# Kernel tuning notes

Hardware: AMD Instinct MI355X
Metric: run time of the kernel (lower is better)

## Reference

```python
import jax, jax.numpy as jnp
import numpy as np

K = 3          # patch_size
PAD = 1        # (K-1)//2
EPS = 1e-8
STYLE_STRENGTH = 1.0


def _whiten(x):
    # WCT whitening: zero-mean, multiply by Cov^{-1/2} (eigendecomposition)
    B, C, H, W = x.shape
    f = x.reshape(B, C, H * W)
    f = f - f.mean(-1, keepdims=True)
    cov = jnp.einsum('bcn,bdn->bcd', f, f) / (H * W - 1)
    e, v = jnp.linalg.eigh(cov)
    d = 1.0 / jnp.sqrt(jnp.maximum(e, EPS))
    wmat = jnp.einsum('bce,be,bde->bcd', v, d, v)   # V diag(e^-1/2) V^T
    return jnp.einsum('bcd,bdn->bcn', wmat, f).reshape(B, C, H, W)


def _color(x, target):
    # WCT coloring: multiply by style Cov^{1/2}, add style mean
    B, C, H, W = x.shape
    f = x.reshape(B, C, H * W)
    t = target.reshape(B, C, -1)
    tm = t.mean(-1, keepdims=True)
    tc = t - tm
    cov = jnp.einsum('bcn,bdn->bcd', tc, tc) / (tc.shape[-1] - 1)
    e, v = jnp.linalg.eigh(cov)
    d = jnp.sqrt(jnp.maximum(e, 0.0))
    cmat = jnp.einsum('bce,be,bde->bcd', v, d, v)   # V diag(e^1/2) V^T
    out = jnp.einsum('bcd,bdn->bcn', cmat, f) + tm
    return out.reshape(B, C, H, W)


def _extract_patches(x):
    # [B,C,H,W] -> [B,H*W,C,K*K], zero padding, stride 1 (matches torch unfold order)
    B, C, H, W = x.shape
    xp = jnp.pad(x, ((0, 0), (0, 0), (PAD, PAD), (PAD, PAD)))
    pats = jnp.stack([xp[:, :, i:i + H, j:j + W] for i in range(K) for j in range(K)], axis=-1)
    return pats.reshape(B, C, H * W, K * K).transpose(0, 2, 1, 3)


def _style_decorator(content_feature, style_feature):
    nc = _whiten(content_feature)
    ns = _whiten(style_feature)
    B, C, H, W = nc.shape
    P = ns.shape[2] * ns.shape[3]                     # number of style patches
    kern = _extract_patches(ns).reshape(B, P, C * K * K)
    knorm = jnp.linalg.norm(kern, axis=2, keepdims=True) + 1e-5
    cpat = _extract_patches(nc).reshape(B, H * W, C * K * K)
    # conv2d with normalized style kernels == cosine-similarity cross-correlation
    score = jnp.einsum('bqm,bpm->bpq', cpat, kern / knorm)    # [B, P, H*W]
    # binarization_patch_score: per-pixel argmax over style patches (one-hot),
    # then deconv with UNNORMALIZED kernels == gather the winning kernel per pixel
    idx = jnp.argmax(score, axis=1)                           # [B, H*W]
    gathered = jnp.take_along_axis(kern, idx[:, :, None], axis=1)  # [B, H*W, C*K*K]
    G = gathered.reshape(B, H, W, C, K, K).transpose(0, 3, 1, 2, 4, 5)  # [B,C,H,W,K,K]
    # conv_transpose2d(pad=K-1) on zero-padded one-hot == overlap-add of kernels
    full = jnp.zeros((B, C, H + K - 1, W + K - 1), dtype=nc.dtype)
    for dx in range(K):
        for dy in range(K):
            full = full.at[:, :, dx:dx + H, dy:dy + W].add(G[..., dx, dy])
    out = full[:, :, PAD:PAD + H, PAD:PAD + W]
    # norm_deconvolution: overlap counts (static)
    nfull = np.zeros((H + K - 1, W + K - 1), dtype=np.float32)
    for dx in range(K):
        for dy in range(K):
            nfull[dx:dx + H, dy:dy + W] += 1.0
    dn = jnp.asarray(nfull[PAD:PAD + H, PAD:PAD + W])
    reassembled = out / dn
    stylized = _color(reassembled, style_feature)
    return (1.0 - STYLE_STRENGTH) * content_feature + STYLE_STRENGTH * stylized


def setup_inputs() -> dict:
    key = jax.random.key(0)
    k1, k2 = jax.random.split(key)
    return {
        'content_feature': jax.random.normal(k1, (2, 512, 64, 64), dtype=jnp.float32),
        'style_feature': jax.random.normal(k2, (2, 512, 64, 64), dtype=jnp.float32),
    }


def reference(content_feature, style_feature):
    return _style_decorator(content_feature, style_feature)
```

## Files before the change

kernel.cpp:

```cpp
#include <hip/hip_runtime.h>


#define CH    512
#define NPIX  4096
#define HPAD  66
#define PPAD  4356
#define MROWS 4480
#define BANDW 2304
#define BANDOFF 2112
#define NS_ITERS 7

typedef unsigned short u16;
typedef _Float16 half8 __attribute__((ext_vector_type(8)));
typedef __attribute__((ext_vector_type(4))) float f32x4;

__device__ __forceinline__ float f16tof(u16 h){
  union { u16 u; _Float16 f; } v; v.u = h; return (float)v.f;
}
__device__ __forceinline__ void split2(float x, u16& h, u16& l){
  _Float16 hf = (_Float16)x;
  float r = (x - (float)hf) * 2048.0f;
  union { u16 u; _Float16 f; } hv, lv;
  hv.f = hf; lv.f = (_Float16)r;
  h = hv.u; l = lv.u;
}
__device__ __forceinline__ void gll16(const void* g, void* l){
  __builtin_amdgcn_global_load_lds((const __attribute__((address_space(1))) unsigned*)g,
                                   (__attribute__((address_space(3))) unsigned*)l,
                                   16, 0, 0);
}
__device__ __forceinline__ f32x4 mfma_f16(half8 a, half8 b, f32x4 c){
  return __builtin_amdgcn_mfma_f32_16x16x32_f16(a, b, c, 0, 0, 0);
}

enum { M_COVP = 0, M_NST = 1, M_X3 = 2, M_WHITEN = 3, M_S0 = 4, M_COLOR = 5 };

struct GP {
  const u16 *Ah, *Al, *Bh, *Bl;
  const u16 *Eh, *El, *Fh, *Fl;
  size_t sAz, sBz;
  float* Cf;
  u16 *Ch, *Cl;
  u16 *Gh, *Gl;
  size_t sCz;
  const float* scales;
  const float* meanv;
  int K;
  int Kit;
};

template<int TILE, int MODE>
__global__ __launch_bounds__(256, 2)
void gemm_sp(GP p){
  constexpr int MF = TILE / 32;
  constexpr bool SYM = (MODE == M_NST) || (MODE == M_X3);
  const int z = blockIdx.z;
  int m0, n0;
  int kbase = 0;
  int za = z, zout = z;
  bool mirror = false;
  if constexpr (MODE == M_COVP){
    const int b = blockIdx.x;
    const int xcd = b & 7, w = b >> 3;
    const int zc = xcd*2 + (w & 1);
    const int tile = w >> 1;
    m0 = (tile >> 3)*64; n0 = (tile & 7)*64;
    kbase = (zc & 3) * p.Kit;
    za = zc >> 2; zout = zc;
  } else if constexpr (SYM){
    int bx = blockIdx.x;
    int ty = 0;
    while((ty+1)*(ty+2)/2 <= bx) ++ty;
    int tx = bx - ty*(ty+1)/2;
    m0 = ty*64; n0 = tx*64; mirror = (tx != ty);
  } else if constexpr (MODE == M_S0){
    const int b = blockIdx.x;
    const int v = (b & 7)*79 + (b >> 3);
    if(v >= 630) return;
    m0 = (v / 18)*128; n0 = (v % 18)*128;
  } else {
    m0 = blockIdx.y*TILE; n0 = blockIdx.x*TILE;
  }

  const u16 *Ah, *Al, *Bh, *Bl;
  if constexpr (MODE == M_X3){
    const size_t zb = (size_t)(z & 3) * CH * CH;
    if(z < 4){ Ah=p.Ah+zb; Al=p.Al+zb; Bh=p.Bh+zb; Bl=p.Bl+zb; }
    else     { Ah=p.Eh+zb; Al=p.El+zb; Bh=p.Fh+zb; Bl=p.Fl+zb; }
  } else {
    Ah = p.Ah + (size_t)za * p.sAz;
    Al = p.Al + (size_t)za * p.sAz;
    Bh = p.Bh + (size_t)za * p.sBz;
    Bl = p.Bl + (size_t)za * p.sBz;
  }

  const int tid = threadIdx.x, ln = tid & 63, wv = tid >> 6;
  const int wm = (wv >> 1) * (TILE/2), wn = (wv & 1) * (TILE/2);
  __shared__ __align__(16) u16 sAh[2][TILE*32], sAl[2][TILE*32];
  __shared__ __align__(16) u16 sBh[2][TILE*32], sBl[2][TILE*32];
  f32x4 acc1[MF][MF], acc2[MF][MF];
#pragma unroll
  for(int i=0;i<MF;++i)
#pragma unroll
    for(int j=0;j<MF;++j){ acc1[i][j] = (f32x4)0.0f; acc2[i][j] = (f32x4)0.0f; }
  const int K = p.K;

  auto stage = [&](int k0, int buf){
#pragma unroll
    for(int s = tid; s < TILE*4; s += 256){
      const int row = s >> 2, pos = s & 3;
      const int kc = pos ^ ((row >> 2) & 3);
      const size_t ga = (size_t)(m0 + row) * K + k0 + kc*8;
      const size_t gb = (size_t)(n0 + row) * K + k0 + kc*8;
      gll16(Ah + ga, sAh[buf] + s*8);
      gll16(Al + ga, sAl[buf] + s*8);
      gll16(Bh + gb, sBh[buf] + s*8);
      gll16(Bl + gb, sBl[buf] + s*8);
    }
  };

  stage(kbase, 0);
  int cur = 0;
  for(int kk = 0; kk < p.Kit; kk += 32){
    __syncthreads();
    if(kk + 32 < p.Kit) stage(kbase + kk + 32, cur ^ 1);
    const u16* pAh = sAh[cur]; const u16* pAl = sAl[cur];
    const u16* pBh = sBh[cur]; const u16* pBl = sBl[cur];
    half8 ah[MF], al[MF], bh[MF], bl[MF];
#pragma unroll
    for(int i=0;i<MF;++i){
      const int ra = wm + i*16 + (ln & 15);
      const int rb = wn + i*16 + (ln & 15);
      const int pa = (ln >> 4) ^ ((ra >> 2) & 3);
      const int pb = (ln >> 4) ^ ((rb >> 2) & 3);
      const int ofa = ra*32 + pa*8;
      const int ofb = rb*32 + pb*8;
      ah[i] = *(const half8*)(pAh + ofa);
      al[i] = *(const half8*)(pAl + ofa);
      bh[i] = *(const half8*)(pBh + ofb);
      bl[i] = *(const half8*)(pBl + ofb);
    }
#pragma unroll
    for(int i=0;i<MF;++i)
#pragma unroll
      for(int j=0;j<MF;++j){
        acc1[i][j] = mfma_f16(ah[i], bh[j], acc1[i][j]);
        acc2[i][j] = mfma_f16(ah[i], bl[j], acc2[i][j]);
        acc2[i][j] = mfma_f16(al[i], bh[j], acc2[i][j]);
      }
    cur ^= 1;
  }
  u16 *C0 = nullptr, *C1 = nullptr;
  if constexpr (MODE == M_NST){
    const size_t zb = (size_t)z * p.sCz;
    C0 = p.Ch + zb; C1 = p.Cl + zb;
  } else if constexpr (MODE == M_X3){
    const size_t zb = (size_t)(z & 3) * p.sCz;
    if(z < 4){ C0 = p.Ch + zb; C1 = p.Cl + zb; }
    else     { C0 = p.Gh + zb; C1 = p.Gl + zb; }
  }
#pragma unroll
  for(int i=0;i<MF;++i)
#pragma unroll
    for(int j=0;j<MF;++j)
#pragma unroll
      for(int r=0;r<4;++r){
        const int m = m0 + wm + i*16 + (ln >> 4)*4 + r;
        const int n = n0 + wn + j*16 + (ln & 15);
        float v = acc1[i][j][r] + acc2[i][j][r] * (1.0f/2048.0f);
        if constexpr (MODE == M_COVP){
          p.Cf[(size_t)zout * p.sCz + (size_t)m * CH + n] = v;
        } else if constexpr (MODE == M_NST || MODE == M_X3){
          if constexpr (MODE == M_NST) v = -0.5f*v + ((m == n) ? 1.5f : 0.0f);
          u16 h, l; split2(v, h, l);
          C0[(size_t)m*CH + n] = h; C1[(size_t)m*CH + n] = l;
          if(mirror){
            C0[(size_t)n*CH + m] = h; C1[(size_t)n*CH + m] = l;
          }
        } else if constexpr (MODE == M_WHITEN){
          v *= p.scales[z*4 + 3];
          const int prow = ((m >> 6) + 1)*HPAD + (m & 63) + 1;
          u16 h, l; split2(v, h, l);
          const size_t o = (size_t)z*p.sCz + (size_t)prow*CH + n;
          p.Ch[o] = h; p.Cl[o] = l;
        } else if constexpr (MODE == M_S0){
          p.Cf[(size_t)m * BANDW + n] = v;
        } else {
          const float sc = p.scales[(2+z)*4 + 2];
          const float mu = p.meanv[(2+z)*CH + m];
          p.Cf[(size_t)z*p.sCz + (size_t)m*NPIX + n] = v*sc + mu;
        }
      }
}

__global__ __launch_bounds__(256)
void cov_reduce_kernel(const float* __restrict__ covp, float* __restrict__ cov){
  size_t t = (size_t)blockIdx.x * 256 + threadIdx.x;
  int z = (int)(t >> 18);
  size_t e = t & 262143;
  float s = 0.f;
#pragma unroll
  for(int c = 0; c < 4; ++c) s += covp[((size_t)(z*4 + c) << 18) + e];
  cov[t] = s * (1.0f / 4095.0f);
}

__global__ __launch_bounds__(256)
void scale_pre_kernel(const float* __restrict__ cov, int* __restrict__ cmax){
  const int z = blockIdx.y;
  const int col = blockIdx.x * 256 + threadIdx.x;
  const float* C = cov + (size_t)z * CH * CH;
  float s = 0.f;
  for(int r = 0; r < CH; ++r) s += fabsf(C[(size_t)r * CH + col]);
  atomicMax(&cmax[z], __float_as_int(s));
}
__global__ __launch_bounds__(64)
void scale_fin_kernel(const int* __restrict__ cmax, float* __restrict__ scales){
  int z = threadIdx.x;
  if(z < 4){
    float c = __int_as_float(cmax[z]);
    scales[z*4+0] = c;
    scales[z*4+1] = 1.0f / c;
    scales[z*4+2] = sqrtf(c);
    scales[z*4+3] = rsqrtf(c);
  }
}

__global__ __launch_bounds__(256)
void mean_kernel(const float* __restrict__ content, const float* __restrict__ style,
                 float* __restrict__ meanv){
  int mm = blockIdx.x;
  int z = mm >> 9, c = mm & 511;
  const float* X = ((z < 2) ? content + (size_t)z * CH * NPIX
                            : style   + (size_t)(z - 2) * CH * NPIX) + (size_t)c * NPIX;
  float s = 0.f;
  for(int i = threadIdx.x; i < NPIX; i += 256) s += X[i];
  __shared__ float red[256];
  red[threadIdx.x] = s; __syncthreads();
  for(int w = 128; w > 0; w >>= 1){
    if(threadIdx.x < w) red[threadIdx.x] += red[threadIdx.x + w];
    __syncthreads();
  }
  if(threadIdx.x == 0) meanv[mm] = red[0] * (1.0f / NPIX);
}

__global__ __launch_bounds__(256)
void center_split_kernel(const float* __restrict__ content, const float* __restrict__ style,
                         const float* __restrict__ meanv,
                         u16* __restrict__ Xch, u16* __restrict__ Xcl,
                         u16* __restrict__ XcTh, u16* __restrict__ XcTl){
  int z = blockIdx.z;
  const float* X = (z < 2) ? content + (size_t)z * CH * NPIX
                           : style   + (size_t)(z - 2) * CH * NPIX;
  int p0 = blockIdx.x * 64, c0 = blockIdx.y * 64;
  __shared__ float T[64][65];
  int col = threadIdx.x & 63, rq = threadIdx.x >> 6;
#pragma unroll
  for(int i = 0; i < 16; ++i){
    int r = i*4 + rq;
    int c = c0 + r;
    float v = X[(size_t)c * NPIX + p0 + col] - meanv[z*CH + c];
    u16 h, l; split2(v, h, l);
    size_t o = (size_t)(z*CH + c) * NPIX + p0 + col;
    Xch[o] = h; Xcl[o] = l;
    T[col][r] = v;
  }
  __syncthreads();
#pragma unroll
  for(int i = 0; i < 16; ++i){
    int r = i*4 + rq;
    float v = T[r][col];
    u16 h, l; split2(v, h, l);
    size_t o = (size_t)(z*NPIX + p0 + r) * CH + c0 + col;
    XcTh[o] = h; XcTl[o] = l;
  }
}

__global__ __launch_bounds__(256)
void ns_init_kernel(const float* __restrict__ cov, const float* __restrict__ scales,
                    u16* Yh, u16* Yl, u16* Zh, u16* Zl){
  size_t t = (size_t)blockIdx.x * 256 + threadIdx.x;
  int z = (int)(t >> 18);
  size_t e = t & 262143;
  int row = (int)(e >> 9), col = (int)(e & 511);
  float v = cov[t] * scales[z*4+1];
  u16 h, l; split2(v, h, l);
  Yh[t] = h; Yl[t] = l;
  Zh[t] = (row == col) ? (u16)0x3C00 : (u16)0;
  Zl[t] = 0;
}

__global__ __launch_bounds__(256)
void cn2_kernel(const u16* __restrict__ Wh, const u16* __restrict__ Wl,
                float* __restrict__ cn2){
  int b = blockIdx.y;
  int row = blockIdx.x * 16 + (threadIdx.x >> 4);
  int t = threadIdx.x & 15;
  float s = 0.f;
  if(row < PPAD){
    size_t base = ((size_t)(2 + b) * MROWS + row) * CH;
    for(int ch = t; ch < 64; ch += 16){
      uint4 hv = *(const uint4*)(Wh + base + ch*8);
      uint4 lv = *(const uint4*)(Wl + base + ch*8);
      const unsigned* hw = (const unsigned*)&hv;
      const unsigned* lw = (const unsigned*)&lv;
#pragma unroll
      for(int w = 0; w < 4; ++w){
        float v0 = f16tof((u16)(hw[w] & 0xFFFF)) + f16tof((u16)(lw[w] & 0xFFFF))*(1.0f/2048.0f);
        float v1 = f16tof((u16)(hw[w] >> 16))    + f16tof((u16)(lw[w] >> 16))*(1.0f/2048.0f);
        s = fmaf(v0, v0, s); s = fmaf(v1, v1, s);
      }
    }
  }
  for(int off = 8; off; off >>= 1) s += __shfl_down(s, off, 16);
  if(t == 0 && row < PPAD) cn2[b*PPAD + row] = s;
}

__global__ __launch_bounds__(256)
void rnorm_kernel(const float* __restrict__ cn2, float* __restrict__ rnorm){
  int b = blockIdx.y;
  int p = blockIdx.x * 256 + threadIdx.x;
  int py = p >> 6, px = p & 63;
  const float* c2 = cn2 + (size_t)b * PPAD + (size_t)py * HPAD + px;
  float s = 0.f;
#pragma unroll
  for(int i = 0; i < 3; ++i)
#pragma unroll
    for(int j = 0; j < 3; ++j) s += c2[i * HPAD + j];
  rnorm[b * 4096 + p] = 1.0f / (sqrtf(s) + 1e-5f);
}

__global__ __launch_bounds__(256)
void score_partial_kernel(const float* __restrict__ S0T, const float* __restrict__ rnorm,
                          float* __restrict__ pmax, int* __restrict__ pidx,
                          int b, int qy0, int colbase){
  const int blk = blockIdx.x;
  const int xcd = blk & 7, w = blk >> 3;
  const int chunk = xcd*8 + (w & 7);
  const int qyb = w >> 3;
  int q = qy0*64 + qyb*256 + threadIdx.x;
  int qy = q >> 6, qx = q & 63;
  int qcol = qy * HPAD + qx - colbase;
  const float* rn = rnorm + b * 4096;
  float best = -1e30f; int bestp = 0;
  for(int p = chunk * 64; p < chunk * 64 + 64; ++p){
    int py = p >> 6, px = p & 63;
    const float* base = S0T + (size_t)(py * HPAD + px) * BANDW + qcol;
    float s = 0.f;
#pragma unroll
    for(int i = 0; i < 3; ++i)
#pragma unroll
      for(int j = 0; j < 3; ++j)
        s += base[(size_t)(i * HPAD + j) * (BANDW + 1)];
    s *= rn[p];
    if(s > best){ best = s; bestp = p; }
  }
  pmax[(size_t)chunk * 4096 + q] = best;
  pidx[(size_t)chunk * 4096 + q] = bestp;
}

__global__ __launch_bounds__(256)
void argmax_merge_kernel(const float* __restrict__ pmax, const int* __restrict__ pidx,
                         int* __restrict__ idx, int b){
  int q = blockIdx.x * 256 + threadIdx.x;
  float best = -1e30f; int bp = 0;
  for(int ch = 0; ch < 64; ++ch){
    float v = pmax[(size_t)ch * 4096 + q];
    if(v > best){ best = v; bp = pidx[(size_t)ch * 4096 + q]; }
  }
  idx[b * 4096 + q] = bp;
}

__global__ __launch_bounds__(256)
void gather_kernel(const u16* __restrict__ Wh, const u16* __restrict__ Wl,
                   const int* __restrict__ idx,
                   u16* __restrict__ RTh, u16* __restrict__ RTl){
  int g = blockIdx.x * 256 + threadIdx.x;
  int cg = g & 63;
  int pix = (g >> 6) & 4095;
  int b = g >> 18;
  int y = pix >> 6, x = pix & 63;
  const int* idxb = idx + b * 4096;
  size_t matbase = (size_t)(2 + b) * MROWS * CH;
  float a8[8] = {0,0,0,0,0,0,0,0};
  int cnt = 0;
#pragma unroll
  for(int i = 0; i < 3; ++i){
    int qy = y + 1 - i;
    if((unsigned)qy >= 64u) continue;
#pragma unroll
    for(int j = 0; j < 3; ++j){
      int qx = x + 1 - j;
      if((unsigned)qx >= 64u) continue;
      int p = idxb[qy * 64 + qx];
      int row = ((p >> 6) + i) * HPAD + (p & 63) + j;
      size_t off = matbase + (size_t)row * CH + cg * 8;
      uint4 hv = *(const uint4*)(Wh + off);
      uint4 lv = *(const uint4*)(Wl + off);
      const unsigned* hw = (const unsigned*)&hv;
      const unsigned* lw = (const unsigned*)&lv;
#pragma unroll
      for(int w = 0; w < 4; ++w){
        a8[2*w]   += f16tof((u16)(hw[w] & 0xFFFF)) + f16tof((u16)(lw[w] & 0xFFFF))*(1.0f/2048.0f);
        a8[2*w+1] += f16tof((u16)(hw[w] >> 16))    + f16tof((u16)(lw[w] >> 16))*(1.0f/2048.0f);
      }
      ++cnt;
    }
  }
  float inv = 1.0f / (float)cnt;
  u16 oh[8], ol[8];
#pragma unroll
  for(int k = 0; k < 8; ++k){
    float v = a8[k] * inv;
    split2(v, oh[k], ol[k]);
  }
  size_t ro = ((size_t)(b * 4096 + pix)) * CH + cg * 8;
  *(uint4*)(RTh + ro) = *(const uint4*)oh;
  *(uint4*)(RTl + ro) = *(const uint4*)ol;
}

extern "C" void kernel_launch(void* const* d_in, const int* in_sizes, int n_in,
                              void* d_out, int out_size, void* d_ws, size_t ws_size,
                              hipStream_t stream){
  (void)in_sizes; (void)n_in; (void)out_size; (void)ws_size;
  const float* content = (const float*)d_in[0];
  const float* style   = (const float*)d_in[1];
  float* out = (float*)d_out;

  char* base = (char*)d_ws;
  size_t off = 0;
  auto take = [&](size_t nbytes) -> char* {
    char* p = base + off;
    off = (off + nbytes + 255) & ~(size_t)255;
    return p;
  };
  const size_t MAT = (size_t)CH*CH*2;
  const size_t FEAT = (size_t)CH*NPIX*2;
  const size_t WMAT = (size_t)MROWS*CH*2;
  const size_t S0SZ = (size_t)MROWS*BANDW*4;

  float* meanv  = (float*)take((size_t)4*CH*sizeof(float));
  float* scales = (float*)take(256);
  int*   cmax   = (int*)  take(256);
  float* cov    = (float*)take((size_t)4*CH*CH*sizeof(float));
  float* covp   = (float*)take((size_t)16*CH*CH*sizeof(float));
  u16 *Yh=(u16*)take(4*MAT), *Yl=(u16*)take(4*MAT);
  u16 *Zh=(u16*)take(4*MAT), *Zl=(u16*)take(4*MAT);
  u16 *Th=(u16*)take(4*MAT), *Tl=(u16*)take(4*MAT);
  u16 *Ynh=(u16*)take(4*MAT), *Ynl=(u16*)take(4*MAT);
  u16 *Znh=(u16*)take(4*MAT), *Znl=(u16*)take(4*MAT);
  char* P1 = take(2*(size_t)4*WMAT);
  u16 *Xch=(u16*)P1, *Xcl=(u16*)(P1+4*FEAT);
  u16 *Wh=(u16*)P1,  *Wl=(u16*)(P1+4*WMAT);
  char* P0 = take(S0SZ);
  u16 *XcTh=(u16*)P0, *XcTl=(u16*)(P0+4*FEAT);
  float* S0T = (float*)P0;
  u16 *RTh=(u16*)P0, *RTl=(u16*)(P0+2*FEAT);
  float* cn2    = (float*)take((size_t)2*PPAD*sizeof(float));
  float* rnormb = (float*)take((size_t)2*4096*sizeof(float));
  float* pmax   = (float*)take((size_t)64*4096*sizeof(float));
  int*   pidx   = (int*)  take((size_t)64*4096*sizeof(int));
  int*   idxb   = (int*)  take((size_t)2*4096*sizeof(int));

  mean_kernel<<<2048, 256, 0, stream>>>(content, style, meanv);
  center_split_kernel<<<dim3(64, 8, 4), 256, 0, stream>>>(content, style, meanv,
                                                          Xch, Xcl, XcTh, XcTl);
  {
    GP g{}; g.Ah=Xch; g.Al=Xcl; g.Bh=Xch; g.Bl=Xcl;
    g.sAz = g.sBz = (size_t)CH*NPIX; g.Cf = covp; g.sCz = (size_t)CH*CH;
    g.K = NPIX; g.Kit = 1024;
    gemm_sp<64, M_COVP><<<dim3(1024), 256, 0, stream>>>(g);
  }
  cov_reduce_kernel<<<4096, 256, 0, stream>>>(covp, cov);
  scale_pre_kernel<<<dim3(2, 4), 256, 0, stream>>>(cov, cmax);
  scale_fin_kernel<<<1, 64, 0, stream>>>(cmax, scales);
  ns_init_kernel<<<4096, 256, 0, stream>>>(cov, scales, Yh, Yl, Zh, Zl);

  u16 *Ach[2]={Yh,Yl}, *Bch[2]={Zh,Zl}, *An[2]={Ynh,Ynl}, *Bn[2]={Znh,Znl};
  for(int it = 0; it < NS_ITERS; ++it){
    GP t{}; t.Ah=Bch[0]; t.Al=Bch[1];
    t.Bh=Ach[0]; t.Bl=Ach[1];
    t.sAz = t.sBz = (size_t)CH*CH; t.Ch=Th; t.Cl=Tl; t.sCz=(size_t)CH*CH;
    t.K = CH; t.Kit = CH;
    gemm_sp<64, M_NST><<<dim3(36, 1, 4), 256, 0, stream>>>(t);
    GP u{}; u.Ah=Ach[0]; u.Al=Ach[1];
    u.Bh=Th; u.Bl=Tl;
    u.Eh=Th; u.El=Tl;
    u.Fh=Bch[0]; u.Fl=Bch[1];
    u.Ch=An[0]; u.Cl=An[1];
    u.Gh=Bn[0]; u.Gl=Bn[1];
    u.sCz=(size_t)CH*CH; u.K = CH; u.Kit = CH;
    gemm_sp<64, M_X3><<<dim3(36, 1, 8), 256, 0, stream>>>(u);
    for(int c = 0; c < 2; ++c){ u16* tmp=Ach[c]; Ach[c]=An[c]; An[c]=tmp;
                                tmp=Bch[c]; Bch[c]=Bn[c]; Bn[c]=tmp; }
  }

  hipMemsetAsync(Wh, 0, 4*WMAT, stream);
  hipMemsetAsync(Wl, 0, 4*WMAT, stream);
  {
    GP w{}; w.Ah=XcTh; w.Al=XcTl; w.sAz=(size_t)NPIX*CH;
    w.Bh=Bch[0]; w.Bl=Bch[1]; w.sBz=(size_t)CH*CH;
    w.Ch=Wh; w.Cl=Wl; w.sCz=(size_t)MROWS*CH; w.scales=scales;
    w.K = CH; w.Kit = CH;
    gemm_sp<128, M_WHITEN><<<dim3(4, 32, 4), 256, 0, stream>>>(w);
  }
  cn2_kernel<<<dim3(273, 2), 256, 0, stream>>>(Wh, Wl, cn2);
  rnorm_kernel<<<dim3(16, 2), 256, 0, stream>>>(cn2, rnormb);

  for(int b = 0; b < 2; ++b){
    for(int band = 0; band < 2; ++band){
      GP s{};
      s.Ah = Wh + (size_t)(2+b)*MROWS*CH; s.Al = Wl + (size_t)(2+b)*MROWS*CH;
      size_t bo = (size_t)b*MROWS*CH + (size_t)(band ? BANDOFF : 0)*CH;
      s.Bh = Wh + bo; s.Bl = Wl + bo;
      s.sAz = s.sBz = 0; s.Cf = S0T; s.sCz = 0; s.K = CH; s.Kit = CH;
      gemm_sp<128, M_S0><<<dim3(632), 256, 0, stream>>>(s);
      score_partial_kernel<<<dim3(512), 256, 0, stream>>>(S0T, rnormb, pmax, pidx,
                                                          b, band ? 32 : 0,
                                                          band ? BANDOFF : 0);
    }
    argmax_merge_kernel<<<16, 256, 0, stream>>>(pmax, pidx, idxb, b);
  }

  gather_kernel<<<2048, 256, 0, stream>>>(Wh, Wl, idxb, RTh, RTl);
  {
    GP c{}; c.Ah = Ach[0] + 2*(size_t)CH*CH; c.Al = Ach[1] + 2*(size_t)CH*CH;
    c.sAz = (size_t)CH*CH;
    c.Bh = RTh; c.Bl = RTl; c.sBz = (size_t)NPIX*CH;
    c.Cf = out; c.sCz = (size_t)CH*NPIX; c.scales = scales; c.meanv = meanv;
    c.K = CH; c.Kit = CH;
    gemm_sp<128, M_COLOR><<<dim3(32, 4, 2), 256, 0, stream>>>(c);
  }
}
```

Before: 872.6 us.

## Merge score bands into one full-width S0 GEMM and fuse cov scale reduction

The two banded S0 GEMM and score passes per batch become a single full-width GEMM (35x35 tiles of 128) writing a 4480-wide S0 buffer, followed by one score kernel that handles two query pixels per thread. The covariance reduce kernel now also accumulates absolute row sums through a block reduction plus atomicAdd, which removes the separate column-scan scale_pre kernel. The covp scratch buffer is aliased onto the Yh region to save memory. The aim is fewer launches and less redundant scan work, at the cost of a larger S0 buffer and a change in summation order through the atomics.

```diff
diff --git a/kernel.cpp b/kernel.cpp
--- a/kernel.cpp
+++ b/kernel.cpp
@@ -6,8 +6,7 @@
 #define HPAD  66
 #define PPAD  4356
 #define MROWS 4480
-#define BANDW 2304
-#define BANDOFF 2112
+#define S0W   4480
 #define NS_ITERS 7
 
 typedef unsigned short u16;
@@ -75,9 +74,9 @@
     m0 = ty*64; n0 = tx*64; mirror = (tx != ty);
   } else if constexpr (MODE == M_S0){
     const int b = blockIdx.x;
-    const int v = (b & 7)*79 + (b >> 3);
-    if(v >= 630) return;
-    m0 = (v / 18)*128; n0 = (v % 18)*128;
+    const int v = (b & 7)*154 + (b >> 3);
+    if(v >= 1225) return;
+    m0 = (v / 35)*128; n0 = (v % 35)*128;
   } else {
     m0 = blockIdx.y*TILE; n0 = blockIdx.x*TILE;
   }
@@ -184,7 +183,7 @@
           const size_t o = (size_t)z*p.sCz + (size_t)prow*CH + n;
           p.Ch[o] = h; p.Cl[o] = l;
         } else if constexpr (MODE == M_S0){
-          p.Cf[(size_t)m * BANDW + n] = v;
+          p.Cf[(size_t)m * S0W + n] = v;
         } else {
           const float sc = p.scales[(2+z)*4 + 2];
           const float mu = p.meanv[(2+z)*CH + m];
@@ -194,34 +193,46 @@
 }
 
 __global__ __launch_bounds__(256)
-void cov_reduce_kernel(const float* __restrict__ covp, float* __restrict__ cov){
+void cov_reduce_kernel(const float* __restrict__ covp, float* __restrict__ cov,
+                       float* __restrict__ rowsum){
   size_t t = (size_t)blockIdx.x * 256 + threadIdx.x;
   int z = (int)(t >> 18);
   size_t e = t & 262143;
   float s = 0.f;
 #pragma unroll
   for(int c = 0; c < 4; ++c) s += covp[((size_t)(z*4 + c) << 18) + e];
-  cov[t] = s * (1.0f / 4095.0f);
-}
-
-__global__ __launch_bounds__(256)
-void scale_pre_kernel(const float* __restrict__ cov, int* __restrict__ cmax){
-  const int z = blockIdx.y;
-  const int col = blockIdx.x * 256 + threadIdx.x;
-  const float* C = cov + (size_t)z * CH * CH;
-  float s = 0.f;
-  for(int r = 0; r < CH; ++r) s += fabsf(C[(size_t)r * CH + col]);
-  atomicMax(&cmax[z], __float_as_int(s));
-}
-__global__ __launch_bounds__(64)
-void scale_fin_kernel(const int* __restrict__ cmax, float* __restrict__ scales){
-  int z = threadIdx.x;
-  if(z < 4){
-    float c = __int_as_float(cmax[z]);
-    scales[z*4+0] = c;
-    scales[z*4+1] = 1.0f / c;
-    scales[z*4+2] = sqrtf(c);
-    scales[z*4+3] = rsqrtf(c);
+  s *= (1.0f / 4095.0f);
+  cov[t] = s;
+  __shared__ float red[256];
+  red[threadIdx.x] = fabsf(s); __syncthreads();
+  for(int w = 128; w > 0; w >>= 1){
+    if(threadIdx.x < w) red[threadIdx.x] += red[threadIdx.x + w];
+    __syncthreads();
+  }
+  if(threadIdx.x == 0){
+    int row = (int)(e >> 9);
+    atomicAdd(&rowsum[z*512 + row], red[0]);
+  }
+}
+
+__global__ __launch_bounds__(256)
+void scale_fin_kernel(const float* __restrict__ rowsum, float* __restrict__ scales){
+  __shared__ float red[256];
+  for(int z = 0; z < 4; ++z){
+    float m = fmaxf(rowsum[z*512 + threadIdx.x], rowsum[z*512 + 256 + threadIdx.x]);
+    red[threadIdx.x] = m; __syncthreads();
+    for(int w = 128; w > 0; w >>= 1){
+      if(threadIdx.x < w) red[threadIdx.x] = fmaxf(red[threadIdx.x], red[threadIdx.x + w]);
+      __syncthreads();
+    }
+    if(threadIdx.x == 0){
+      float c = red[0];
+      scales[z*4+0] = c;
+      scales[z*4+1] = 1.0f / c;
+      scales[z*4+2] = sqrtf(c);
+      scales[z*4+3] = rsqrtf(c);
+    }
+    __syncthreads();
   }
 }
 
@@ -331,31 +342,35 @@
 
 __global__ __launch_bounds__(256)
 void score_partial_kernel(const float* __restrict__ S0T, const float* __restrict__ rnorm,
-                          float* __restrict__ pmax, int* __restrict__ pidx,
-                          int b, int qy0, int colbase){
+                          float* __restrict__ pmax, int* __restrict__ pidx, int b){
   const int blk = blockIdx.x;
   const int xcd = blk & 7, w = blk >> 3;
   const int chunk = xcd*8 + (w & 7);
-  const int qyb = w >> 3;
-  int q = qy0*64 + qyb*256 + threadIdx.x;
-  int qy = q >> 6, qx = q & 63;
-  int qcol = qy * HPAD + qx - colbase;
+  const int qg = w >> 3;
+  const int t = threadIdx.x;
+  const int q0 = qg*512 + t, q1 = q0 + 256;
+  const int qc0 = (q0 >> 6)*HPAD + (q0 & 63);
+  const int qc1 = (q1 >> 6)*HPAD + (q1 & 63);
   const float* rn = rnorm + b * 4096;
-  float best = -1e30f; int bestp = 0;
-  for(int p = chunk * 64; p < chunk * 64 + 64; ++p){
-    int py = p >> 6, px = p & 63;
-    const float* base = S0T + (size_t)(py * HPAD + px) * BANDW + qcol;
-    float s = 0.f;
+  float b0 = -1e30f, b1 = -1e30f; int i0 = 0, i1 = 0;
+  for(int p = chunk*64; p < chunk*64 + 64; ++p){
+    const size_t base = (size_t)((p >> 6)*HPAD + (p & 63)) * S0W;
+    float s0 = 0.f, s1 = 0.f;
 #pragma unroll
     for(int i = 0; i < 3; ++i)
 #pragma unroll
-      for(int j = 0; j < 3; ++j)
-        s += base[(size_t)(i * HPAD + j) * (BANDW + 1)];
-    s *= rn[p];
-    if(s > best){ best = s; bestp = p; }
-  }
-  pmax[(size_t)chunk * 4096 + q] = best;
-  pidx[(size_t)chunk * 4096 + q] = bestp;
+      for(int j = 0; j < 3; ++j){
+        const size_t d = (size_t)(i*HPAD + j) * (S0W + 1);
+        s0 += S0T[base + qc0 + d];
+        s1 += S0T[base + qc1 + d];
+      }
+    const float r = rn[p];
+    s0 *= r; s1 *= r;
+    if(s0 > b0){ b0 = s0; i0 = p; }
+    if(s1 > b1){ b1 = s1; i1 = p; }
+  }
+  pmax[(size_t)chunk*4096 + q0] = b0; pidx[(size_t)chunk*4096 + q0] = i0;
+  pmax[(size_t)chunk*4096 + q1] = b1; pidx[(size_t)chunk*4096 + q1] = i1;
 }
 
 __global__ __launch_bounds__(256)
@@ -436,18 +451,18 @@
   const size_t MAT = (size_t)CH*CH*2;
   const size_t FEAT = (size_t)CH*NPIX*2;
   const size_t WMAT = (size_t)MROWS*CH*2;
-  const size_t S0SZ = (size_t)MROWS*BANDW*4;
+  const size_t S0SZ = (size_t)MROWS*S0W*4;
 
   float* meanv  = (float*)take((size_t)4*CH*sizeof(float));
   float* scales = (float*)take(256);
-  int*   cmax   = (int*)  take(256);
+  float* rowsum = (float*)take((size_t)4*CH*sizeof(float));
   float* cov    = (float*)take((size_t)4*CH*CH*sizeof(float));
-  float* covp   = (float*)take((size_t)16*CH*CH*sizeof(float));
   u16 *Yh=(u16*)take(4*MAT), *Yl=(u16*)take(4*MAT);
   u16 *Zh=(u16*)take(4*MAT), *Zl=(u16*)take(4*MAT);
   u16 *Th=(u16*)take(4*MAT), *Tl=(u16*)take(4*MAT);
   u16 *Ynh=(u16*)take(4*MAT), *Ynl=(u16*)take(4*MAT);
   u16 *Znh=(u16*)take(4*MAT), *Znl=(u16*)take(4*MAT);
+  float* covp = (float*)Yh;
   char* P1 = take(2*(size_t)4*WMAT);
   u16 *Xch=(u16*)P1, *Xcl=(u16*)(P1+4*FEAT);
   u16 *Wh=(u16*)P1,  *Wl=(u16*)(P1+4*WMAT);
@@ -461,6 +476,8 @@
   int*   pidx   = (int*)  take((size_t)64*4096*sizeof(int));
   int*   idxb   = (int*)  take((size_t)2*4096*sizeof(int));
 
+  hipMemsetAsync(rowsum, 0, (size_t)4*CH*sizeof(float), stream);
+
   mean_kernel<<<2048, 256, 0, stream>>>(content, style, meanv);
   center_split_kernel<<<dim3(64, 8, 4), 256, 0, stream>>>(content, style, meanv,
                                                           Xch, Xcl, XcTh, XcTl);
@@ -470,9 +487,8 @@
     g.K = NPIX; g.Kit = 1024;
     gemm_sp<64, M_COVP><<<dim3(1024), 256, 0, stream>>>(g);
   }
-  cov_reduce_kernel<<<4096, 256, 0, stream>>>(covp, cov);
-  scale_pre_kernel<<<dim3(2, 4), 256, 0, stream>>>(cov, cmax);
-  scale_fin_kernel<<<1, 64, 0, stream>>>(cmax, scales);
+  cov_reduce_kernel<<<4096, 256, 0, stream>>>(covp, cov, rowsum);
+  scale_fin_kernel<<<1, 256, 0, stream>>>(rowsum, scales);
   ns_init_kernel<<<4096, 256, 0, stream>>>(cov, scales, Yh, Yl, Zh, Zl);
 
   u16 *Ach[2]={Yh,Yl}, *Bch[2]={Zh,Zl}, *An[2]={Ynh,Ynl}, *Bn[2]={Znh,Znl};
@@ -507,17 +523,12 @@
   rnorm_kernel<<<dim3(16, 2), 256, 0, stream>>>(cn2, rnormb);
 
   for(int b = 0; b < 2; ++b){
-    for(int band = 0; band < 2; ++band){
-      GP s{};
-      s.Ah = Wh + (size_t)(2+b)*MROWS*CH; s.Al = Wl + (size_t)(2+b)*MROWS*CH;
-      size_t bo = (size_t)b*MROWS*CH + (size_t)(band ? BANDOFF : 0)*CH;
-      s.Bh = Wh + bo; s.Bl = Wl + bo;
-      s.sAz = s.sBz = 0; s.Cf = S0T; s.sCz = 0; s.K = CH; s.Kit = CH;
-      gemm_sp<128, M_S0><<<dim3(632), 256, 0, stream>>>(s);
-      score_partial_kernel<<<dim3(512), 256, 0, stream>>>(S0T, rnormb, pmax, pidx,
-                                                          b, band ? 32 : 0,
-                                                          band ? BANDOFF : 0);
-    }
+    GP s{};
+    s.Ah = Wh + (size_t)(2+b)*MROWS*CH; s.Al = Wl + (size_t)(2+b)*MROWS*CH;
+    s.Bh = Wh + (size_t)b*MROWS*CH;     s.Bl = Wl + (size_t)b*MROWS*CH;
+    s.sAz = s.sBz = 0; s.Cf = S0T; s.sCz = 0; s.K = CH; s.Kit = CH;
+    gemm_sp<128, M_S0><<<dim3(1232), 256, 0, stream>>>(s);
+    score_partial_kernel<<<dim3(512), 256, 0, stream>>>(S0T, rnormb, pmax, pidx, b);
     argmax_merge_kernel<<<16, 256, 0, stream>>>(pmax, pidx, idxb, b);
   }
 
```

Measured after the change: 786.7 us. 9.8% less time.
